# Kernel tuning notes

Hardware: AMD Instinct MI355X
Metric: run time of the kernel (lower is better)

The kernel has to match this reference:

```python
import jax, jax.numpy as jnp
import numpy as np

L, D = 2048, 1024
D_INNER = 2 * D          # expand=2
D_STATE = 16
D_CONV = 4
DT_RANK = D // 16        # ceil(1024/16) = 64
HID = 4 * D
EPS = 1e-5


def _layernorm(x, g, b):
    mu = jnp.mean(x, axis=-1, keepdims=True)
    var = jnp.mean(jnp.square(x - mu), axis=-1, keepdims=True)
    return (x - mu) * jax.lax.rsqrt(var + EPS) * g + b


def setup_inputs() -> dict:
    key = jax.random.key(0)
    ks = jax.random.split(key, 12)
    f = lambda k, sh, s=0.02: (jax.random.normal(k, sh, jnp.float32) * s)
    return {
        "x": jax.random.normal(ks[0], (L, D), jnp.float32),
        "ln1_g": jnp.ones((D,), jnp.float32),
        "ln1_b": jnp.zeros((D,), jnp.float32),
        "ln2_g": jnp.ones((D,), jnp.float32),
        "ln2_b": jnp.zeros((D,), jnp.float32),
        "in_proj_w": f(ks[1], (2 * D_INNER, D)),
        "conv_w": f(ks[2], (D_INNER, D_CONV), 0.1),
        "conv_b": jnp.zeros((D_INNER,), jnp.float32),
        "x_proj_w": f(ks[3], (DT_RANK + 2 * D_STATE, D_INNER)),
        "dt_proj_w": f(ks[4], (D_INNER, DT_RANK), 0.1),
        "dt_proj_b": f(ks[5], (D_INNER,), 0.1),
        "A_log": jnp.log(jnp.broadcast_to(
            jnp.arange(1, D_STATE + 1, dtype=jnp.float32), (D_INNER, D_STATE))),
        "D_param": jnp.ones((D_INNER,), jnp.float32),
        "out_proj_w": f(ks[6], (D, D_INNER)),
        "ffn_w1": f(ks[7], (HID, D)),
        "ffn_b1": jnp.zeros((HID,), jnp.float32),
        "ffn_w2": f(ks[8], (D, HID)),
        "ffn_b2": jnp.zeros((D,), jnp.float32),
    }


def _mamba(x, in_proj_w, conv_w, conv_b, x_proj_w, dt_proj_w, dt_proj_b,
           A_log, D_param, out_proj_w):
    # x: (L, D)
    xz = x @ in_proj_w.T                    # (L, 2*d_inner)
    xm, z = xz[:, :D_INNER], xz[:, D_INNER:]
    # causal depthwise conv1d, kernel d_conv, output length L
    xp = jnp.pad(xm, ((D_CONV - 1, 0), (0, 0)))
    xc = conv_b
    for k in range(D_CONV):                 # 4 taps, fixed small loop
        xc = xc + xp[k:k + L] * conv_w[None, :, k]
    xc = jax.nn.silu(xc)                    # (L, d_inner)
    proj = xc @ x_proj_w.T                  # (L, dt_rank + 2*d_state)
    dt = proj[:, :DT_RANK]
    B = proj[:, DT_RANK:DT_RANK + D_STATE]  # (L, d_state)
    C = proj[:, DT_RANK + D_STATE:]         # (L, d_state)
    delta = jax.nn.softplus(dt @ dt_proj_w.T + dt_proj_b)  # (L, d_inner)
    A = -jnp.exp(A_log)                     # (d_inner, d_state)
    dA = jnp.exp(delta[:, :, None] * A[None])               # (L, d_inner, d_state)
    dBx = delta[:, :, None] * B[:, None, :] * xc[:, :, None]

    def step(h, inp):
        dA_t, dBx_t, C_t = inp
        h = h * dA_t + dBx_t                # (d_inner, d_state)
        y = jnp.einsum('ds,s->d', h, C_t)
        return h, y

    h0 = jnp.zeros((D_INNER, D_STATE), x.dtype)
    _, ys = jax.lax.scan(step, h0, (dA, dBx, C))            # ys: (L, d_inner)
    y = ys + xc * D_param
    y = y * jax.nn.silu(z)
    return y @ out_proj_w.T                 # (L, D)


def reference(x, ln1_g, ln1_b, ln2_g, ln2_b, in_proj_w, conv_w, conv_b,
              x_proj_w, dt_proj_w, dt_proj_b, A_log, D_param, out_proj_w,
              ffn_w1, ffn_b1, ffn_w2, ffn_b2):
    residual = x
    h = _layernorm(x, ln1_g, ln1_b)
    h = _mamba(h, in_proj_w, conv_w, conv_b, x_proj_w, dt_proj_w, dt_proj_b,
               A_log, D_param, out_proj_w)
    h = h + residual
    # FFN has an internal residual around the normed input, plus outer residual
    n = _layernorm(h, ln2_g, ln2_b)
    f = n + (jax.nn.relu(n @ ffn_w1.T + ffn_b1) @ ffn_w2.T + ffn_b2)
    return h + f
```

## Files before the change

### kernel.cpp

```cpp
#include <hip/hip_runtime.h>
#include <hip/hip_bf16.h>
#include <math.h>

#define L_SEQ 2048
#define DMODEL 1024
#define DINNER 2048
#define DSTATE 16
#define DTRANK 64
#define NHID 4096
#define NC 64
#define LC 32

typedef __bf16 bf16_t;
typedef __bf16 bf16x4 __attribute__((ext_vector_type(4)));
typedef __bf16 bf16x8 __attribute__((ext_vector_type(8)));
typedef float f32x4 __attribute__((ext_vector_type(4)));

#define WAIT_VM0 0x0F70
#define WAIT_VM4 0x0F74
#define WAIT_VM8 0x0F78

__device__ __forceinline__ void async_cp16(const bf16_t* g, bf16_t* l) {
    __builtin_amdgcn_global_load_lds(
        (const __attribute__((address_space(1))) void*)g,
        (__attribute__((address_space(3))) void*)l, 16, 0, 0);
}

template <int EPI, int OUTBF16>
__global__ __launch_bounds__(256) void gemm_async(
    const bf16_t* __restrict__ A, int lda,
    const bf16_t* __restrict__ W, int ldw,
    void* __restrict__ Cv, int ldc,
    int N, int Kslice, long cstride,
    const float* __restrict__ bias)
{
    __shared__ bf16_t As[4 * 4096];
    __shared__ bf16_t Ws[4 * 4096];

    const int tid  = threadIdx.x;
    const int lane = tid & 63;
    const int w    = tid >> 6;
    const int m0   = blockIdx.y * 128;
    const int n0   = blockIdx.x * 128;
    const int kz   = blockIdx.z;
    const int k0   = kz * Kslice;

    const int p   = lane & 3;
    const int r0  = 2 * w * 16 + (lane >> 2);
    const int r1  = r0 + 16;
    const int dc0 = (p - ((r0 >> 1) & 3)) & 3;
    const int dc1 = (p - ((r1 >> 1) & 3)) & 3;

    const bf16_t* gA0 = A + (size_t)(m0 + r0) * lda + k0 + dc0 * 8;
    const bf16_t* gA1 = A + (size_t)(m0 + r1) * lda + k0 + dc1 * 8;
    int gn0 = n0 + r0; if (gn0 > N - 1) gn0 = N - 1;
    int gn1 = n0 + r1; if (gn1 > N - 1) gn1 = N - 1;
    const bf16_t* gW0 = W + (size_t)gn0 * ldw + k0 + dc0 * 8;
    const bf16_t* gW1 = W + (size_t)gn1 * ldw + k0 + dc1 * 8;

    const int lo0 = (2 * w) * 512;
    const int lo1 = lo0 + 512;

    const int wr   = w >> 1;
    const int wc   = w & 1;
    const int quad = lane >> 4;
    const int lr   = lane & 15;
    int offA[4], offW[4];
    #pragma unroll
    for (int i = 0; i < 4; ++i) {
        int ra = wr * 64 + i * 16 + lr;
        offA[i] = ra * 32 + (((quad + ((ra >> 1) & 3)) & 3) * 8);
        int rb = wc * 64 + i * 16 + lr;
        offW[i] = rb * 32 + (((quad + ((rb >> 1) & 3)) & 3) * 8);
    }

    const int niter = Kslice >> 5;

    #pragma unroll
    for (int j = 0; j < 3; ++j) {
        if (j < niter) {
            int sb = j * 4096;
            async_cp16(gA0, &As[sb + lo0]);
            async_cp16(gA1, &As[sb + lo1]);
            async_cp16(gW0, &Ws[sb + lo0]);
            async_cp16(gW1, &Ws[sb + lo1]);
            gA0 += 32; gA1 += 32; gW0 += 32; gW1 += 32;
        }
    }

    f32x4 acc[4][4] = {};
    for (int it = 0; it < niter; ++it) {
        if (it + 3 <= niter)      __builtin_amdgcn_s_waitcnt(WAIT_VM8);
        else if (it + 2 <= niter) __builtin_amdgcn_s_waitcnt(WAIT_VM4);
        else                      __builtin_amdgcn_s_waitcnt(WAIT_VM0);
        __builtin_amdgcn_s_barrier();
        asm volatile("" ::: "memory");

        if (it + 3 < niter) {
            int sb = ((it + 3) & 3) * 4096;
            async_cp16(gA0, &As[sb + lo0]);
            async_cp16(gA1, &As[sb + lo1]);
            async_cp16(gW0, &Ws[sb + lo0]);
            async_cp16(gW1, &Ws[sb + lo1]);
            gA0 += 32; gA1 += 32; gW0 += 32; gW1 += 32;
        }

        const int cb = (it & 3) * 4096;
        bf16x8 af[4], bw[4];
        #pragma unroll
        for (int i = 0; i < 4; ++i) af[i] = *(const bf16x8*)&As[cb + offA[i]];
        #pragma unroll
        for (int j = 0; j < 4; ++j) bw[j] = *(const bf16x8*)&Ws[cb + offW[j]];
        #pragma unroll
        for (int i = 0; i < 4; ++i)
            #pragma unroll
            for (int j = 0; j < 4; ++j)
                acc[i][j] = __builtin_amdgcn_mfma_f32_16x16x32_bf16(af[i], bw[j], acc[i][j], 0, 0, 0);
    }

    float*  Cf = (float*)Cv + (size_t)kz * cstride;
    bf16_t* Cb = (bf16_t*)Cv + (size_t)kz * cstride;
    #pragma unroll
    for (int i = 0; i < 4; ++i) {
        int row0 = m0 + wr * 64 + i * 16 + quad * 4;
        #pragma unroll
        for (int j = 0; j < 4; ++j) {
            int col = n0 + wc * 64 + j * 16 + lr;
            if (col < N) {
                float bv = (EPI == 2 || EPI == 3) ? bias[col] : 0.f;
                #pragma unroll
                for (int r = 0; r < 4; ++r) {
                    float v = acc[i][j][r];
                    if (EPI == 2) v = fmaxf(v + bv, 0.f);
                    else if (EPI == 3) {
                        float t = v + bv;
                        v = fmaxf(t, 0.f) + log1pf(__expf(-fabsf(t)));
                    }
                    size_t o = (size_t)(row0 + r) * ldc + col;
                    if (OUTBF16) Cb[o] = (bf16_t)v;
                    else         Cf[o] = v;
                }
            }
        }
    }
}

__global__ __launch_bounds__(256) void cvt_weights(
    const float* __restrict__ s0, const float* __restrict__ s1,
    const float* __restrict__ s2, const float* __restrict__ s3,
    const float* __restrict__ s4, const float* __restrict__ s5,
    bf16_t* __restrict__ dst)
{
    int e = (blockIdx.x * 256 + threadIdx.x) * 4;
    const float* src; int local;
    if      (e < 4194304)  { src = s0; local = e; }
    else if (e < 4390912)  { src = s1; local = e - 4194304; }
    else if (e < 4521984)  { src = s2; local = e - 4390912; }
    else if (e < 6619136)  { src = s3; local = e - 4521984; }
    else if (e < 10813440) { src = s4; local = e - 6619136; }
    else                   { src = s5; local = e - 10813440; }
    float4 v = *(const float4*)(src + local);
    bf16x4 o;
    o[0] = (bf16_t)v.x; o[1] = (bf16_t)v.y; o[2] = (bf16_t)v.z; o[3] = (bf16_t)v.w;
    *(bf16x4*)(dst + e) = o;
}

template <int MODE>
__global__ __launch_bounds__(256) void ln_kernel(
    const float* __restrict__ x, const float* __restrict__ g,
    const float* __restrict__ b, float* __restrict__ outf,
    bf16_t* __restrict__ outb)
{
    const int row = blockIdx.x;
    const float* xr = x + (size_t)row * DMODEL;
    float v[4];
    float s = 0.f, sq = 0.f;
    #pragma unroll
    for (int i = 0; i < 4; ++i) {
        v[i] = xr[threadIdx.x + i * 256];
        s += v[i]; sq += v[i] * v[i];
    }
    #pragma unroll
    for (int off = 32; off > 0; off >>= 1) {
        s += __shfl_xor(s, off); sq += __shfl_xor(sq, off);
    }
    __shared__ float rs_[4], rq_[4];
    int w = threadIdx.x >> 6;
    if ((threadIdx.x & 63) == 0) { rs_[w] = s; rq_[w] = sq; }
    __syncthreads();
    s  = rs_[0] + rs_[1] + rs_[2] + rs_[3];
    sq = rq_[0] + rq_[1] + rq_[2] + rq_[3];
    float mu  = s * (1.f / DMODEL);
    float var = sq * (1.f / DMODEL) - mu * mu;
    float rsd = rsqrtf(var + 1e-5f);
    #pragma unroll
    for (int i = 0; i < 4; ++i) {
        int col = threadIdx.x + i * 256;
        float o = (v[i] - mu) * rsd * g[col] + b[col];
        if (MODE == 1) outf[(size_t)row * DMODEL + col] = o;
        outb[(size_t)row * DMODEL + col] = (bf16_t)o;
    }
}

__global__ __launch_bounds__(256) void conv_silu(
    const bf16_t* __restrict__ xz, const float* __restrict__ cw,
    const float* __restrict__ cb, bf16_t* __restrict__ xc)
{
    int gid = blockIdx.x * 256 + threadIdx.x;
    int c = gid & (DINNER - 1);
    int t = gid >> 11;
    float acc = cb[c];
    #pragma unroll
    for (int k = 0; k < 4; ++k) {
        int tt = t + k - 3;
        if (tt >= 0) acc += (float)xz[(size_t)tt * (2 * DINNER) + c] * cw[c * 4 + k];
    }
    float sig = 1.f / (1.f + __expf(-acc));
    xc[gid] = (bf16_t)(acc * sig);
}

__global__ __launch_bounds__(256) void scan_pass1(
    const float* __restrict__ delta, const bf16_t* __restrict__ xc,
    const float* __restrict__ proj, const float* __restrict__ A_log,
    float* __restrict__ carryH, float* __restrict__ sumd)
{
    const int c = blockIdx.x;
    const int d = blockIdx.y * 256 + threadIdx.x;
    const int t0 = c * LC;

    __shared__ float Bs[LC][DSTATE];
    for (int i = threadIdx.x; i < LC * DSTATE; i += 256) {
        int tt = i >> 4, s = i & 15;
        Bs[tt][s] = proj[(size_t)(t0 + tt) * 96 + DTRANK + s];
    }
    __syncthreads();

    float a[DSTATE], h[DSTATE];
    #pragma unroll
    for (int s = 0; s < DSTATE; ++s) {
        a[s] = -__expf(A_log[d * DSTATE + s]);
        h[s] = 0.f;
    }
    float sd = 0.f;
    for (int i = 0; i < LC; ++i) {
        int t = t0 + i;
        float dl = delta[(size_t)t * DINNER + d];
        float x  = (float)xc[(size_t)t * DINNER + d];
        sd += dl;
        float dx = dl * x;
        #pragma unroll
        for (int s = 0; s < DSTATE; ++s)
            h[s] = h[s] * __expf(dl * a[s]) + dx * Bs[i][s];
    }
    #pragma unroll
    for (int s = 0; s < DSTATE; ++s)
        carryH[((size_t)c * DINNER + d) * DSTATE + s] = h[s];
    sumd[c * DINNER + d] = sd;
}

__global__ __launch_bounds__(256) void scan_pass2(
    const float* __restrict__ A_log, const float* __restrict__ carryH,
    const float* __restrict__ sumd, float* __restrict__ hinit)
{
    int idx = blockIdx.x * 256 + threadIdx.x;
    int d = idx >> 4;
    float a = -__expf(A_log[idx]);
    float hc = 0.f;
    for (int c = 0; c < NC; ++c) {
        hinit[(size_t)c * (DINNER * DSTATE) + idx] = hc;
        float P = __expf(a * sumd[c * DINNER + d]);
        hc = carryH[(size_t)c * (DINNER * DSTATE) + idx] + P * hc;
    }
}

__global__ __launch_bounds__(256) void scan_pass3(
    const float* __restrict__ delta, const bf16_t* __restrict__ xc,
    const float* __restrict__ proj, const float* __restrict__ A_log,
    const float* __restrict__ hinit, const float* __restrict__ Dp,
    const bf16_t* __restrict__ xz, bf16_t* __restrict__ yact)
{
    const int c = blockIdx.x;
    const int d = blockIdx.y * 256 + threadIdx.x;
    const int t0 = c * LC;

    __shared__ float Bs[LC][DSTATE], Cs[LC][DSTATE];
    for (int i = threadIdx.x; i < LC * DSTATE; i += 256) {
        int tt = i >> 4, s = i & 15;
        size_t base = (size_t)(t0 + tt) * 96;
        Bs[tt][s] = proj[base + DTRANK + s];
        Cs[tt][s] = proj[base + DTRANK + DSTATE + s];
    }
    __syncthreads();

    float a[DSTATE], h[DSTATE];
    #pragma unroll
    for (int s = 0; s < DSTATE; ++s) {
        a[s] = -__expf(A_log[d * DSTATE + s]);
        h[s] = hinit[(size_t)c * (DINNER * DSTATE) + d * DSTATE + s];
    }
    float DD = Dp[d];
    for (int i = 0; i < LC; ++i) {
        int t = t0 + i;
        float dl = delta[(size_t)t * DINNER + d];
        float x  = (float)xc[(size_t)t * DINNER + d];
        float dx = dl * x;
        float y = 0.f;
        #pragma unroll
        for (int s = 0; s < DSTATE; ++s) {
            h[s] = h[s] * __expf(dl * a[s]) + dx * Bs[i][s];
            y += h[s] * Cs[i][s];
        }
        float yv = y + x * DD;
        float z = (float)xz[(size_t)t * (2 * DINNER) + DINNER + d];
        float sil = z / (1.f + __expf(-z));
        yact[(size_t)t * DINNER + d] = (bf16_t)(yv * sil);
    }
}

__global__ __launch_bounds__(256) void reduce4(
    const float* __restrict__ part, float* __restrict__ proj,
    bf16_t* __restrict__ projdt)
{
    int i = blockIdx.x * 256 + threadIdx.x;
    float v = 0.f;
    #pragma unroll
    for (int s = 0; s < 16; ++s) v += part[(size_t)s * 196608 + i];
    proj[i] = v;
    int row = i / 96;
    int col = i - row * 96;
    if (col < DTRANK) projdt[row * DTRANK + col] = (bf16_t)v;
}

__global__ __launch_bounds__(256) void reduce9(
    const bf16_t* __restrict__ part, const float* __restrict__ x,
    float* __restrict__ hres)
{
    int i = (blockIdx.x * 256 + threadIdx.x) * 4;
    float4 c = *(const float4*)(x + i);
    float s0 = c.x, s1 = c.y, s2 = c.z, s3 = c.w;
    #pragma unroll
    for (int sl = 0; sl < 4; ++sl) {
        bf16x4 v = *(const bf16x4*)(part + (size_t)sl * 2097152 + i);
        s0 += (float)v[0]; s1 += (float)v[1]; s2 += (float)v[2]; s3 += (float)v[3];
    }
    *(float4*)(hres + i) = make_float4(s0, s1, s2, s3);
}

__global__ __launch_bounds__(256) void reduce12(
    const bf16_t* __restrict__ part, const float* __restrict__ b2,
    const float* __restrict__ hres, const float* __restrict__ nbuf,
    float* __restrict__ out)
{
    int i = (blockIdx.x * 256 + threadIdx.x) * 4;
    float4 bb = *(const float4*)(b2 + (i & (DMODEL - 1)));
    float4 h  = *(const float4*)(hres + i);
    float4 n  = *(const float4*)(nbuf + i);
    float s0 = bb.x + h.x + n.x, s1 = bb.y + h.y + n.y;
    float s2 = bb.z + h.z + n.z, s3 = bb.w + h.w + n.w;
    #pragma unroll
    for (int sl = 0; sl < 4; ++sl) {
        bf16x4 v = *(const bf16x4*)(part + (size_t)sl * 2097152 + i);
        s0 += (float)v[0]; s1 += (float)v[1]; s2 += (float)v[2]; s3 += (float)v[3];
    }
    *(float4*)(out + i) = make_float4(s0, s1, s2, s3);
}

extern "C" void kernel_launch(void* const* d_in, const int* in_sizes, int n_in,
                              void* d_out, int out_size, void* d_ws, size_t ws_size,
                              hipStream_t stream)
{
    const float* x        = (const float*)d_in[0];
    const float* ln1_g    = (const float*)d_in[1];
    const float* ln1_b    = (const float*)d_in[2];
    const float* ln2_g    = (const float*)d_in[3];
    const float* ln2_b    = (const float*)d_in[4];
    const float* in_proj  = (const float*)d_in[5];
    const float* conv_w   = (const float*)d_in[6];
    const float* conv_b   = (const float*)d_in[7];
    const float* x_proj   = (const float*)d_in[8];
    const float* dt_proj  = (const float*)d_in[9];
    const float* dt_b     = (const float*)d_in[10];
    const float* A_log    = (const float*)d_in[11];
    const float* D_param  = (const float*)d_in[12];
    const float* out_proj = (const float*)d_in[13];
    const float* ffn_w1   = (const float*)d_in[14];
    const float* ffn_b1   = (const float*)d_in[15];
    const float* ffn_w2   = (const float*)d_in[16];
    const float* ffn_b2   = (const float*)d_in[17];
    float* out = (float*)d_out;

    char* base = (char*)d_ws;
    bf16_t* Wb     = (bf16_t*)(base);
    bf16_t* w_inp  = Wb;
    bf16_t* w_xp   = Wb + 4194304;
    bf16_t* w_dtp  = Wb + 4390912;
    bf16_t* w_outp = Wb + 4521984;
    bf16_t* w_f1   = Wb + 6619136;
    bf16_t* w_f2   = Wb + 10813440;

    bf16_t* h1b    = (bf16_t*)(base + 30015488);
    float*  proj   = (float*)(base + 30015488);
    bf16_t* projdt = (bf16_t*)(base + 30015488 + 786432);
    bf16_t* xz     = (bf16_t*)(base + 34209792);
    bf16_t* ffnh   = xz;
    bf16_t* xc     = (bf16_t*)(base + 50987008);
    float*  part   = (float*)(base + 59375616);
    float*  delta  = part;
    bf16_t* partb  = (bf16_t*)part;
    float*  carry  = (float*)(base + 76152832);
    bf16_t* nbufb  = (bf16_t*)carry;
    float*  sumd   = (float*)(base + 84541440);
    float*  hinit  = (float*)(base + 85065728);
    float*  nbuf   = hinit;
    bf16_t* yact   = (bf16_t*)(base + 93454336);
    float*  hres   = (float*)(base + 101842944);

    cvt_weights<<<14656, 256, 0, stream>>>(in_proj, x_proj, dt_proj, out_proj,
                                           ffn_w1, ffn_w2, Wb);
    ln_kernel<0><<<L_SEQ, 256, 0, stream>>>(x, ln1_g, ln1_b, nullptr, h1b);
    gemm_async<0, 1><<<dim3(32, 16, 1), 256, 0, stream>>>(
        h1b, DMODEL, w_inp, DMODEL, xz, 4096, 4096, 1024, 0, nullptr);
    conv_silu<<<(L_SEQ * DINNER) / 256, 256, 0, stream>>>(xz, conv_w, conv_b, xc);
    gemm_async<0, 0><<<dim3(1, 16, 16), 256, 0, stream>>>(
        xc, DINNER, w_xp, DINNER, part, 96, 96, 128, 196608L, nullptr);
    reduce4<<<768, 256, 0, stream>>>(part, proj, projdt);
    gemm_async<3, 0><<<dim3(16, 16, 1), 256, 0, stream>>>(
        projdt, DTRANK, w_dtp, DTRANK, delta, DINNER, DINNER, DTRANK, 0, dt_b);
    scan_pass1<<<dim3(NC, DINNER / 256), 256, 0, stream>>>(delta, xc, proj, A_log, carry, sumd);
    scan_pass2<<<(DINNER * DSTATE) / 256, 256, 0, stream>>>(A_log, carry, sumd, hinit);
    scan_pass3<<<dim3(NC, DINNER / 256), 256, 0, stream>>>(delta, xc, proj, A_log, hinit,
                                                           D_param, xz, yact);
    gemm_async<0, 1><<<dim3(8, 16, 4), 256, 0, stream>>>(
        yact, DINNER, w_outp, DINNER, partb, DMODEL, DMODEL, 512, 2097152L, nullptr);
    reduce9<<<2048, 256, 0, stream>>>(partb, x, hres);
    ln_kernel<1><<<L_SEQ, 256, 0, stream>>>(hres, ln2_g, ln2_b, nbuf, nbufb);
    gemm_async<2, 1><<<dim3(32, 16, 1), 256, 0, stream>>>(
        nbufb, DMODEL, w_f1, DMODEL, ffnh, NHID, NHID, 1024, 0, ffn_b1);
    gemm_async<0, 1><<<dim3(8, 16, 4), 256, 0, stream>>>(
        ffnh, NHID, w_f2, NHID, partb, DMODEL, DMODEL, 1024, 2097152L, nullptr);
    reduce12<<<2048, 256, 0, stream>>>(partb, ffn_b2, hres, nbuf, out);
}
```

Before: 379.1 us.

## Fuse weight convert with LN1, split-K reduce with LN2, swizzle GEMM blocks, bf16 delta

Weight conversion and the first layernorm now run in one launch, and the out-proj split-K reduction is fused with the second layernorm, which removes two launches and one full read/write of the residual. A block-index swizzle is added to the two large 32x16-grid GEMMs to improve L2 reuse of A and W tiles. Delta is stored as bf16 instead of fp32, halving its traffic in both scan passes at some cost in precision. The scan_pass2 carry loop is batched so eight chunk loads are issued before the serial recurrence.

```diff
diff --git a/kernel.cpp b/kernel.cpp
--- a/kernel.cpp
+++ b/kernel.cpp
@@ -26,7 +26,7 @@
         (__attribute__((address_space(3))) void*)l, 16, 0, 0);
 }
 
-template <int EPI, int OUTBF16>
+template <int EPI, int OUTBF16, int SWZ>
 __global__ __launch_bounds__(256) void gemm_async(
     const bf16_t* __restrict__ A, int lda,
     const bf16_t* __restrict__ W, int ldw,
@@ -40,8 +40,16 @@
     const int tid  = threadIdx.x;
     const int lane = tid & 63;
     const int w    = tid >> 6;
-    const int m0   = blockIdx.y * 128;
-    const int n0   = blockIdx.x * 128;
+
+    int bx = blockIdx.x, by = blockIdx.y;
+    if (SWZ == 1) {
+        int lid = by * 32 + bx;
+        int r = lid & 7, i = lid >> 3;
+        bx = (r & 3) * 8 + (i & 7);
+        by = (r >> 2) * 8 + (i >> 3);
+    }
+    const int m0   = by * 128;
+    const int n0   = bx * 128;
     const int kz   = blockIdx.z;
     const int k0   = kz * Kslice;
 
@@ -145,33 +153,30 @@
     }
 }
 
-__global__ __launch_bounds__(256) void cvt_weights(
+__global__ __launch_bounds__(256) void cvt_ln1(
     const float* __restrict__ s0, const float* __restrict__ s1,
     const float* __restrict__ s2, const float* __restrict__ s3,
     const float* __restrict__ s4, const float* __restrict__ s5,
-    bf16_t* __restrict__ dst)
-{
-    int e = (blockIdx.x * 256 + threadIdx.x) * 4;
-    const float* src; int local;
-    if      (e < 4194304)  { src = s0; local = e; }
-    else if (e < 4390912)  { src = s1; local = e - 4194304; }
-    else if (e < 4521984)  { src = s2; local = e - 4390912; }
-    else if (e < 6619136)  { src = s3; local = e - 4521984; }
-    else if (e < 10813440) { src = s4; local = e - 6619136; }
-    else                   { src = s5; local = e - 10813440; }
-    float4 v = *(const float4*)(src + local);
-    bf16x4 o;
-    o[0] = (bf16_t)v.x; o[1] = (bf16_t)v.y; o[2] = (bf16_t)v.z; o[3] = (bf16_t)v.w;
-    *(bf16x4*)(dst + e) = o;
-}
-
-template <int MODE>
-__global__ __launch_bounds__(256) void ln_kernel(
+    bf16_t* __restrict__ dst,
     const float* __restrict__ x, const float* __restrict__ g,
-    const float* __restrict__ b, float* __restrict__ outf,
-    bf16_t* __restrict__ outb)
-{
-    const int row = blockIdx.x;
+    const float* __restrict__ b, bf16_t* __restrict__ outb)
+{
+    if (blockIdx.x < 14656) {
+        int e = (blockIdx.x * 256 + threadIdx.x) * 4;
+        const float* src; int local;
+        if      (e < 4194304)  { src = s0; local = e; }
+        else if (e < 4390912)  { src = s1; local = e - 4194304; }
+        else if (e < 4521984)  { src = s2; local = e - 4390912; }
+        else if (e < 6619136)  { src = s3; local = e - 4521984; }
+        else if (e < 10813440) { src = s4; local = e - 6619136; }
+        else                   { src = s5; local = e - 10813440; }
+        float4 v = *(const float4*)(src + local);
+        bf16x4 o;
+        o[0] = (bf16_t)v.x; o[1] = (bf16_t)v.y; o[2] = (bf16_t)v.z; o[3] = (bf16_t)v.w;
+        *(bf16x4*)(dst + e) = o;
+        return;
+    }
+    const int row = blockIdx.x - 14656;
     const float* xr = x + (size_t)row * DMODEL;
     float v[4];
     float s = 0.f, sq = 0.f;
@@ -196,9 +201,7 @@
     #pragma unroll
     for (int i = 0; i < 4; ++i) {
         int col = threadIdx.x + i * 256;
-        float o = (v[i] - mu) * rsd * g[col] + b[col];
-        if (MODE == 1) outf[(size_t)row * DMODEL + col] = o;
-        outb[(size_t)row * DMODEL + col] = (bf16_t)o;
+        outb[(size_t)row * DMODEL + col] = (bf16_t)((v[i] - mu) * rsd * g[col] + b[col]);
     }
 }
 
@@ -220,7 +223,7 @@
 }
 
 __global__ __launch_bounds__(256) void scan_pass1(
-    const float* __restrict__ delta, const bf16_t* __restrict__ xc,
+    const bf16_t* __restrict__ delta, const bf16_t* __restrict__ xc,
     const float* __restrict__ proj, const float* __restrict__ A_log,
     float* __restrict__ carryH, float* __restrict__ sumd)
 {
@@ -244,7 +247,7 @@
     float sd = 0.f;
     for (int i = 0; i < LC; ++i) {
         int t = t0 + i;
-        float dl = delta[(size_t)t * DINNER + d];
+        float dl = (float)delta[(size_t)t * DINNER + d];
         float x  = (float)xc[(size_t)t * DINNER + d];
         sd += dl;
         float dx = dl * x;
@@ -266,15 +269,23 @@
     int d = idx >> 4;
     float a = -__expf(A_log[idx]);
     float hc = 0.f;
-    for (int c = 0; c < NC; ++c) {
-        hinit[(size_t)c * (DINNER * DSTATE) + idx] = hc;
-        float P = __expf(a * sumd[c * DINNER + d]);
-        hc = carryH[(size_t)c * (DINNER * DSTATE) + idx] + P * hc;
+    for (int c0 = 0; c0 < NC; c0 += 8) {
+        float H[8], P[8];
+        #pragma unroll
+        for (int j = 0; j < 8; ++j) {
+            H[j] = carryH[(size_t)(c0 + j) * (DINNER * DSTATE) + idx];
+            P[j] = __expf(a * sumd[(c0 + j) * DINNER + d]);
+        }
+        #pragma unroll
+        for (int j = 0; j < 8; ++j) {
+            hinit[(size_t)(c0 + j) * (DINNER * DSTATE) + idx] = hc;
+            hc = H[j] + P[j] * hc;
+        }
     }
 }
 
 __global__ __launch_bounds__(256) void scan_pass3(
-    const float* __restrict__ delta, const bf16_t* __restrict__ xc,
+    const bf16_t* __restrict__ delta, const bf16_t* __restrict__ xc,
     const float* __restrict__ proj, const float* __restrict__ A_log,
     const float* __restrict__ hinit, const float* __restrict__ Dp,
     const bf16_t* __restrict__ xz, bf16_t* __restrict__ yact)
@@ -301,7 +312,7 @@
     float DD = Dp[d];
     for (int i = 0; i < LC; ++i) {
         int t = t0 + i;
-        float dl = delta[(size_t)t * DINNER + d];
+        float dl = (float)delta[(size_t)t * DINNER + d];
         float x  = (float)xc[(size_t)t * DINNER + d];
         float dx = dl * x;
         float y = 0.f;
@@ -331,19 +342,46 @@
     if (col < DTRANK) projdt[row * DTRANK + col] = (bf16_t)v;
 }
 
-__global__ __launch_bounds__(256) void reduce9(
+__global__ __launch_bounds__(256) void red9_ln2(
     const bf16_t* __restrict__ part, const float* __restrict__ x,
-    float* __restrict__ hres)
-{
-    int i = (blockIdx.x * 256 + threadIdx.x) * 4;
-    float4 c = *(const float4*)(x + i);
-    float s0 = c.x, s1 = c.y, s2 = c.z, s3 = c.w;
-    #pragma unroll
-    for (int sl = 0; sl < 4; ++sl) {
-        bf16x4 v = *(const bf16x4*)(part + (size_t)sl * 2097152 + i);
-        s0 += (float)v[0]; s1 += (float)v[1]; s2 += (float)v[2]; s3 += (float)v[3];
-    }
-    *(float4*)(hres + i) = make_float4(s0, s1, s2, s3);
+    const float* __restrict__ g, const float* __restrict__ b,
+    float* __restrict__ hres, float* __restrict__ nbuf,
+    bf16_t* __restrict__ nbufb)
+{
+    const int row = blockIdx.x;
+    const size_t base = (size_t)row * DMODEL;
+    float v[4];
+    float s = 0.f, sq = 0.f;
+    #pragma unroll
+    for (int i = 0; i < 4; ++i) {
+        int col = threadIdx.x + i * 256;
+        float acc = x[base + col];
+        #pragma unroll
+        for (int sl = 0; sl < 4; ++sl)
+            acc += (float)part[(size_t)sl * 2097152 + base + col];
+        hres[base + col] = acc;
+        v[i] = acc; s += acc; sq += acc * acc;
+    }
+    #pragma unroll
+    for (int off = 32; off > 0; off >>= 1) {
+        s += __shfl_xor(s, off); sq += __shfl_xor(sq, off);
+    }
+    __shared__ float rs_[4], rq_[4];
+    int w = threadIdx.x >> 6;
+    if ((threadIdx.x & 63) == 0) { rs_[w] = s; rq_[w] = sq; }
+    __syncthreads();
+    s  = rs_[0] + rs_[1] + rs_[2] + rs_[3];
+    sq = rq_[0] + rq_[1] + rq_[2] + rq_[3];
+    float mu  = s * (1.f / DMODEL);
+    float var = sq * (1.f / DMODEL) - mu * mu;
+    float rsd = rsqrtf(var + 1e-5f);
+    #pragma unroll
+    for (int i = 0; i < 4; ++i) {
+        int col = threadIdx.x + i * 256;
+        float o = (v[i] - mu) * rsd * g[col] + b[col];
+        nbuf[base + col] = o;
+        nbufb[base + col] = (bf16_t)o;
+    }
 }
 
 __global__ __launch_bounds__(256) void reduce12(
@@ -405,7 +443,7 @@
     bf16_t* ffnh   = xz;
     bf16_t* xc     = (bf16_t*)(base + 50987008);
     float*  part   = (float*)(base + 59375616);
-    float*  delta  = part;
+    bf16_t* delta  = (bf16_t*)part;
     bf16_t* partb  = (bf16_t*)part;
     float*  carry  = (float*)(base + 76152832);
     bf16_t* nbufb  = (bf16_t*)carry;
@@ -415,28 +453,27 @@
     bf16_t* yact   = (bf16_t*)(base + 93454336);
     float*  hres   = (float*)(base + 101842944);
 
-    cvt_weights<<<14656, 256, 0, stream>>>(in_proj, x_proj, dt_proj, out_proj,
-                                           ffn_w1, ffn_w2, Wb);
-    ln_kernel<0><<<L_SEQ, 256, 0, stream>>>(x, ln1_g, ln1_b, nullptr, h1b);
-    gemm_async<0, 1><<<dim3(32, 16, 1), 256, 0, stream>>>(
+    cvt_ln1<<<14656 + 2048, 256, 0, stream>>>(in_proj, x_proj, dt_proj, out_proj,
+                                              ffn_w1, ffn_w2, Wb,
+                                              x, ln1_g, ln1_b, h1b);
+    gemm_async<0, 1, 1><<<dim3(32, 16, 1), 256, 0, stream>>>(
         h1b, DMODEL, w_inp, DMODEL, xz, 4096, 4096, 1024, 0, nullptr);
     conv_silu<<<(L_SEQ * DINNER) / 256, 256, 0, stream>>>(xz, conv_w, conv_b, xc);
-    gemm_async<0, 0><<<dim3(1, 16, 16), 256, 0, stream>>>(
+    gemm_async<0, 0, 0><<<dim3(1, 16, 16), 256, 0, stream>>>(
         xc, DINNER, w_xp, DINNER, part, 96, 96, 128, 196608L, nullptr);
     reduce4<<<768, 256, 0, stream>>>(part, proj, projdt);
-    gemm_async<3, 0><<<dim3(16, 16, 1), 256, 0, stream>>>(
+    gemm_async<3, 1, 0><<<dim3(16, 16, 1), 256, 0, stream>>>(
         projdt, DTRANK, w_dtp, DTRANK, delta, DINNER, DINNER, DTRANK, 0, dt_b);
     scan_pass1<<<dim3(NC, DINNER / 256), 256, 0, stream>>>(delta, xc, proj, A_log, carry, sumd);
     scan_pass2<<<(DINNER * DSTATE) / 256, 256, 0, stream>>>(A_log, carry, sumd, hinit);
     scan_pass3<<<dim3(NC, DINNER / 256), 256, 0, stream>>>(delta, xc, proj, A_log, hinit,
                                                            D_param, xz, yact);
-    gemm_async<0, 1><<<dim3(8, 16, 4), 256, 0, stream>>>(
+    gemm_async<0, 1, 0><<<dim3(8, 16, 4), 256, 0, stream>>>(
         yact, DINNER, w_outp, DINNER, partb, DMODEL, DMODEL, 512, 2097152L, nullptr);
-    reduce9<<<2048, 256, 0, stream>>>(partb, x, hres);
-    ln_kernel<1><<<L_SEQ, 256, 0, stream>>>(hres, ln2_g, ln2_b, nbuf, nbufb);
-    gemm_async<2, 1><<<dim3(32, 16, 1), 256, 0, stream>>>(
+    red9_ln2<<<L_SEQ, 256, 0, stream>>>(partb, x, ln2_g, ln2_b, hres, nbuf, nbufb);
+    gemm_async<2, 1, 1><<<dim3(32, 16, 1), 256, 0, stream>>>(
         nbufb, DMODEL, w_f1, DMODEL, ffnh, NHID, NHID, 1024, 0, ffn_b1);
-    gemm_async<0, 1><<<dim3(8, 16, 4), 256, 0, stream>>>(
+    gemm_async<0, 1, 0><<<dim3(8, 16, 4), 256, 0, stream>>>(
         ffnh, NHID, w_f2, NHID, partb, DMODEL, DMODEL, 1024, 2097152L, nullptr);
     reduce12<<<2048, 256, 0, stream>>>(partb, ffn_b2, hres, nbuf, out);
 }
```

Result: faster. 371.6 us (-2.0%).
